# Kernel tuning notes

Hardware: AMD Instinct MI355X
Metric: run time of the kernel (lower is better)

## Reference

```python
import jax, jax.numpy as jnp
import numpy as np

N_NODES = 50000
N_EDGES = 800000
D_FEAT = 128
D_EMB = 128


def setup_inputs() -> dict:
    key = jax.random.key(0)
    k1, k2, k3, k4, k5 = jax.random.split(key, 5)
    feature = jax.random.normal(k1, (N_NODES, D_FEAT), dtype=jnp.float32)
    edge_src = jax.random.randint(k2, (N_EDGES,), 0, N_NODES, dtype=jnp.int32)
    edge_dst = jax.random.randint(k3, (N_EDGES,), 0, N_NODES, dtype=jnp.int32)
    edge_w = jax.random.uniform(k4, (N_EDGES,), dtype=jnp.float32)
    # reset_parameters: uniform(-stdv, stdv), stdv = 1/sqrt(embedding_size)
    stdv = 1.0 / np.sqrt(D_EMB)
    weight = jax.random.uniform(k5, (D_FEAT, D_EMB), dtype=jnp.float32,
                                minval=-stdv, maxval=stdv)
    return {"feature": feature, "edge_src": edge_src, "edge_dst": edge_dst,
            "edge_w": edge_w, "weight": weight}


def reference(feature, edge_src, edge_dst, edge_w, weight):
    # spmm(adj, feature): out[dst] += w * feature[src]
    msgs = edge_w[:, None] * feature[edge_src]          # [E, D_FEAT]
    agg = jax.ops.segment_sum(msgs, edge_dst, num_segments=feature.shape[0])
    # residual blend then dense projection
    blended = 0.5 * agg + 0.5 * feature                  # [N, D_FEAT]
    return blended @ weight                              # [N, D_EMB]
```

## Files before the change

kernel.cpp:

```cpp
#include <hip/hip_runtime.h>

#define N_NODES 50000
#define N_EDGES 800000
#define D 128
#define NBUCK 196
#define CAP 4800
#define CHUNK 2048

typedef __attribute__((ext_vector_type(8))) short short8;
typedef __attribute__((ext_vector_type(4))) float f32x4;

__device__ __forceinline__ unsigned short f2bf(float f) {
    unsigned u = __float_as_uint(f);
    u += 0x7fff + ((u >> 16) & 1);
    return (unsigned short)(u >> 16);
}

__global__ __launch_bounds__(256) void prep(const float2* __restrict__ feat2,
                                            unsigned* __restrict__ fb,
                                            const float* __restrict__ W,
                                            unsigned short* __restrict__ Wt,
                                            int* __restrict__ gcur) {
    int blk = blockIdx.x, t = threadIdx.x;
    if (blk < 12500) {
        int i = blk * 256 + t;
        float2 f = feat2[i];
        fb[i] = (unsigned)f2bf(f.x) | ((unsigned)f2bf(f.y) << 16);
    } else if (blk < 12564) {
        int idx = (blk - 12500) * 256 + t;
        int n = idx >> 7, k = idx & 127;
        Wt[idx] = f2bf(W[k * 128 + n]);
    } else {
        if (t < NBUCK) gcur[t] = 0;
    }
}

__global__ __launch_bounds__(256) void passA(const int* __restrict__ esrc,
                                             const int* __restrict__ edst,
                                             const float* __restrict__ ew,
                                             int* __restrict__ gcur,
                                             uint2* __restrict__ tmp) {
    __shared__ int lh[NBUCK], lbase[NBUCK], lcur[NBUCK];
    int t = threadIdx.x;
    for (int i = t; i < NBUCK; i += 256) lh[i] = 0;
    __syncthreads();

    int e0 = blockIdx.x * CHUNK;
    int s[8], d[8];
    float w[8];
#pragma unroll
    for (int j = 0; j < 8; ++j) {
        int e = e0 + j * 256 + t;
        if (e < N_EDGES) {
            s[j] = esrc[e]; d[j] = edst[e]; w[j] = ew[e];
            atomicAdd(&lh[d[j] >> 8], 1);
        } else d[j] = -1;
    }
    __syncthreads();
    for (int i = t; i < NBUCK; i += 256) {
        lbase[i] = atomicAdd(&gcur[i], lh[i]);
        lcur[i] = 0;
    }
    __syncthreads();
#pragma unroll
    for (int j = 0; j < 8; ++j) {
        if (d[j] >= 0) {
            int b = d[j] >> 8;
            int r = atomicAdd(&lcur[b], 1);
            tmp[(size_t)b * CAP + lbase[b] + r] =
                make_uint2((unsigned)s[j] | ((unsigned)(d[j] & 255) << 16),
                           __float_as_uint(w[j]));
        }
    }
}

__global__ __launch_bounds__(256) void passB(const int* __restrict__ gcur,
                                             const uint2* __restrict__ tmp,
                                             int* __restrict__ offsets,
                                             uint2* __restrict__ sw) {
    __shared__ int gb[NBUCK];
    __shared__ int hist[256], ps[256];
    __shared__ int sbase;
    int b = blockIdx.x, t = threadIdx.x;
    for (int i = t; i < NBUCK; i += 256) gb[i] = gcur[i];
    hist[t] = 0;
    __syncthreads();
    if (t == 0) {
        int run = 0;
        for (int i = 0; i < b; ++i) run += gb[i];
        sbase = run;
    }
    __syncthreads();
    int base = sbase, cnt = gb[b];
    const uint2* seg = tmp + (size_t)b * CAP;

    for (int i = t; i < cnt; i += 256) atomicAdd(&hist[seg[i].x >> 16], 1);
    __syncthreads();
    int h = hist[t];
    ps[t] = h;
    __syncthreads();
    for (int off = 1; off < 256; off <<= 1) {
        int x = (t >= off) ? ps[t - off] : 0;
        __syncthreads();
        ps[t] += x;
        __syncthreads();
    }
    int o = base + ps[t] - h;
    int node = b * 256 + t;
    if (node < N_NODES) offsets[node] = o;
    if (b == NBUCK - 1 && t == 0) offsets[N_NODES] = N_EDGES;
    __syncthreads();
    hist[t] = o;
    __syncthreads();
    for (int i = t; i < cnt; i += 256) {
        uint2 u = seg[i];
        int pos = atomicAdd(&hist[u.x >> 16], 1);
        sw[pos] = make_uint2(u.x & 0xffffu, u.y);
    }
}

__global__ __launch_bounds__(256) void aggregate_bf16(const int* __restrict__ offsets,
                                                      const uint2* __restrict__ sw,
                                                      const unsigned* __restrict__ fb,
                                                      float* __restrict__ out) {
    int n = blockIdx.x * 4 + (threadIdx.x >> 6);
    n = __builtin_amdgcn_readfirstlane(n);
    int lane = threadIdx.x & 63;
    int b = offsets[n], e2 = offsets[n + 1];
    float ax = 0.f, ay = 0.f;
    int e = b;
    for (; e + 4 <= e2; e += 4) {
        uint2 p0 = sw[e], p1 = sw[e + 1], p2 = sw[e + 2], p3 = sw[e + 3];
        unsigned u0 = fb[(size_t)p0.x * 64 + lane];
        unsigned u1 = fb[(size_t)p1.x * 64 + lane];
        unsigned u2 = fb[(size_t)p2.x * 64 + lane];
        unsigned u3 = fb[(size_t)p3.x * 64 + lane];
        float w0 = __uint_as_float(p0.y), w1 = __uint_as_float(p1.y);
        float w2 = __uint_as_float(p2.y), w3 = __uint_as_float(p3.y);
        ax += w0 * __uint_as_float(u0 << 16);
        ay += w0 * __uint_as_float(u0 & 0xffff0000u);
        ax += w1 * __uint_as_float(u1 << 16);
        ay += w1 * __uint_as_float(u1 & 0xffff0000u);
        ax += w2 * __uint_as_float(u2 << 16);
        ay += w2 * __uint_as_float(u2 & 0xffff0000u);
        ax += w3 * __uint_as_float(u3 << 16);
        ay += w3 * __uint_as_float(u3 & 0xffff0000u);
    }
    for (; e < e2; ++e) {
        uint2 p = sw[e];
        unsigned u = fb[(size_t)p.x * 64 + lane];
        float w = __uint_as_float(p.y);
        ax += w * __uint_as_float(u << 16);
        ay += w * __uint_as_float(u & 0xffff0000u);
    }
    unsigned us = fb[(size_t)n * 64 + lane];
    float sx = __uint_as_float(us << 16), sy = __uint_as_float(us & 0xffff0000u);
    ((float2*)out)[(size_t)n * 64 + lane] = make_float2(0.5f * (ax + sx), 0.5f * (ay + sy));
}

__global__ __launch_bounds__(256) void gemm_mfma_inplace(const unsigned short* __restrict__ Wt,
                                                         float* __restrict__ out) {
    int wave = threadIdx.x >> 6;
    int lane = threadIdx.x & 63;
    int quad = lane >> 4;
    int col  = lane & 15;
    int m0 = blockIdx.x * 64 + wave * 16;
    int rowA = m0 + col;
    int r = rowA < N_NODES ? rowA : N_NODES - 1;
    const float* rp = out + (size_t)r * D;

    short8 a[4];
#pragma unroll
    for (int kk = 0; kk < 4; ++kk) {
        int k0 = kk * 32 + quad * 8;
        float4 lo = *reinterpret_cast<const float4*>(rp + k0);
        float4 hi = *reinterpret_cast<const float4*>(rp + k0 + 4);
        short8 av;
        av[0] = (short)f2bf(lo.x); av[1] = (short)f2bf(lo.y);
        av[2] = (short)f2bf(lo.z); av[3] = (short)f2bf(lo.w);
        av[4] = (short)f2bf(hi.x); av[5] = (short)f2bf(hi.y);
        av[6] = (short)f2bf(hi.z); av[7] = (short)f2bf(hi.w);
        a[kk] = av;
    }

#pragma unroll
    for (int n0 = 0; n0 < 8; ++n0) {
        const short8* bp = reinterpret_cast<const short8*>(Wt) + ((n0 * 16 + col) * 16 + quad);
        f32x4 acc = {0.f, 0.f, 0.f, 0.f};
        acc = __builtin_amdgcn_mfma_f32_16x16x32_bf16(a[0], bp[0],  acc, 0, 0, 0);
        acc = __builtin_amdgcn_mfma_f32_16x16x32_bf16(a[1], bp[4],  acc, 0, 0, 0);
        acc = __builtin_amdgcn_mfma_f32_16x16x32_bf16(a[2], bp[8],  acc, 0, 0, 0);
        acc = __builtin_amdgcn_mfma_f32_16x16x32_bf16(a[3], bp[12], acc, 0, 0, 0);
#pragma unroll
        for (int rr = 0; rr < 4; ++rr) {
            int grow = m0 + quad * 4 + rr;
            if (grow < N_NODES) out[(size_t)grow * D + n0 * 16 + col] = acc[rr];
        }
    }
}

extern "C" void kernel_launch(void* const* d_in, const int* in_sizes, int n_in,
                              void* d_out, int out_size, void* d_ws, size_t ws_size,
                              hipStream_t stream) {
    const float* feat = (const float*)d_in[0];
    const int*   esrc = (const int*)d_in[1];
    const int*   edst = (const int*)d_in[2];
    const float* ew   = (const float*)d_in[3];
    const float* W    = (const float*)d_in[4];
    float*       out  = (float*)d_out;

    char* ws = (char*)d_ws;
    uint2*          sw      = (uint2*)(ws + 0);
    unsigned*       fb      = (unsigned*)(ws + 6400000);
    int*            offsets = (int*)(ws + 19200000);
    unsigned short* Wt      = (unsigned short*)(ws + 19400064);
    int*            gcur    = (int*)(ws + 19432832);
    uint2* tmp = (uint2*)d_out;

    prep<<<12565, 256, 0, stream>>>((const float2*)feat, fb, W, Wt, gcur);
    passA<<<(N_EDGES + CHUNK - 1) / CHUNK, 256, 0, stream>>>(esrc, edst, ew, gcur, tmp);
    passB<<<NBUCK, 256, 0, stream>>>(gcur, tmp, offsets, sw);
    aggregate_bf16<<<N_NODES / 4, 256, 0, stream>>>(offsets, sw, fb, out);
    gemm_mfma_inplace<<<(N_NODES + 63) / 64, 256, 0, stream>>>(Wt, out);
}
```

Before: 170.2 us.

## Fuse aggregation with MFMA projection and merge prep into bucketing pass

Aggregation and the bf16 MFMA projection are merged into one kernel. Each block aggregates 16 rows into an LDS tile as bf16, then four waves each compute two 16-column output tiles, so the fp32 intermediate no longer makes a round trip through global memory. The prep and passA kernels are merged into one launch, with counter zeroing moved to a memset, and the gather loop is unrolled to 8 edges for more loads in flight. In exchange there is less parallelism per row in the aggregation, and each block has to wait at a barrier before its projection can start.

```diff
diff --git a/kernel.cpp b/kernel.cpp
--- a/kernel.cpp
+++ b/kernel.cpp
@@ -6,6 +6,9 @@
 #define NBUCK 196
 #define CAP 4800
 #define CHUNK 2048
+#define PA_BLKS ((N_EDGES + CHUNK - 1) / CHUNK)
+#define FB_BLKS 12500
+#define WT_BLKS 64
 
 typedef __attribute__((ext_vector_type(8))) short short8;
 typedef __attribute__((ext_vector_type(4))) float f32x4;
@@ -16,36 +19,32 @@
     return (unsigned short)(u >> 16);
 }
 
-__global__ __launch_bounds__(256) void prep(const float2* __restrict__ feat2,
-                                            unsigned* __restrict__ fb,
-                                            const float* __restrict__ W,
-                                            unsigned short* __restrict__ Wt,
-                                            int* __restrict__ gcur) {
+__global__ __launch_bounds__(256) void prep_passA(
+    const float2* __restrict__ feat2, unsigned* __restrict__ fb,
+    const float* __restrict__ W, unsigned short* __restrict__ Wt,
+    const int* __restrict__ esrc, const int* __restrict__ edst,
+    const float* __restrict__ ew, int* __restrict__ gcur,
+    uint2* __restrict__ tmp) {
+    __shared__ int lh[NBUCK], lbase[NBUCK], lcur[NBUCK];
     int blk = blockIdx.x, t = threadIdx.x;
-    if (blk < 12500) {
-        int i = blk * 256 + t;
-        float2 f = feat2[i];
-        fb[i] = (unsigned)f2bf(f.x) | ((unsigned)f2bf(f.y) << 16);
-    } else if (blk < 12564) {
-        int idx = (blk - 12500) * 256 + t;
-        int n = idx >> 7, k = idx & 127;
-        Wt[idx] = f2bf(W[k * 128 + n]);
-    } else {
-        if (t < NBUCK) gcur[t] = 0;
-    }
-}
-
-__global__ __launch_bounds__(256) void passA(const int* __restrict__ esrc,
-                                             const int* __restrict__ edst,
-                                             const float* __restrict__ ew,
-                                             int* __restrict__ gcur,
-                                             uint2* __restrict__ tmp) {
-    __shared__ int lh[NBUCK], lbase[NBUCK], lcur[NBUCK];
-    int t = threadIdx.x;
+
+    if (blk >= PA_BLKS) {
+        int b2 = blk - PA_BLKS;
+        if (b2 < FB_BLKS) {
+            int i = b2 * 256 + t;
+            float2 f = feat2[i];
+            fb[i] = (unsigned)f2bf(f.x) | ((unsigned)f2bf(f.y) << 16);
+        } else {
+            int idx = (b2 - FB_BLKS) * 256 + t;
+            int n = idx >> 7, k = idx & 127;
+            Wt[idx] = f2bf(W[k * 128 + n]);
+        }
+        return;
+    }
+
     for (int i = t; i < NBUCK; i += 256) lh[i] = 0;
     __syncthreads();
-
-    int e0 = blockIdx.x * CHUNK;
+    int e0 = blk * CHUNK;
     int s[8], d[8];
     float w[8];
 #pragma unroll
@@ -119,72 +118,61 @@
     }
 }
 
-__global__ __launch_bounds__(256) void aggregate_bf16(const int* __restrict__ offsets,
-                                                      const uint2* __restrict__ sw,
-                                                      const unsigned* __restrict__ fb,
-                                                      float* __restrict__ out) {
-    int n = blockIdx.x * 4 + (threadIdx.x >> 6);
-    n = __builtin_amdgcn_readfirstlane(n);
-    int lane = threadIdx.x & 63;
-    int b = offsets[n], e2 = offsets[n + 1];
-    float ax = 0.f, ay = 0.f;
-    int e = b;
-    for (; e + 4 <= e2; e += 4) {
-        uint2 p0 = sw[e], p1 = sw[e + 1], p2 = sw[e + 2], p3 = sw[e + 3];
-        unsigned u0 = fb[(size_t)p0.x * 64 + lane];
-        unsigned u1 = fb[(size_t)p1.x * 64 + lane];
-        unsigned u2 = fb[(size_t)p2.x * 64 + lane];
-        unsigned u3 = fb[(size_t)p3.x * 64 + lane];
-        float w0 = __uint_as_float(p0.y), w1 = __uint_as_float(p1.y);
-        float w2 = __uint_as_float(p2.y), w3 = __uint_as_float(p3.y);
-        ax += w0 * __uint_as_float(u0 << 16);
-        ay += w0 * __uint_as_float(u0 & 0xffff0000u);
-        ax += w1 * __uint_as_float(u1 << 16);
-        ay += w1 * __uint_as_float(u1 & 0xffff0000u);
-        ax += w2 * __uint_as_float(u2 << 16);
-        ay += w2 * __uint_as_float(u2 & 0xffff0000u);
-        ax += w3 * __uint_as_float(u3 << 16);
-        ay += w3 * __uint_as_float(u3 & 0xffff0000u);
-    }
-    for (; e < e2; ++e) {
-        uint2 p = sw[e];
-        unsigned u = fb[(size_t)p.x * 64 + lane];
-        float w = __uint_as_float(p.y);
-        ax += w * __uint_as_float(u << 16);
-        ay += w * __uint_as_float(u & 0xffff0000u);
-    }
-    unsigned us = fb[(size_t)n * 64 + lane];
-    float sx = __uint_as_float(us << 16), sy = __uint_as_float(us & 0xffff0000u);
-    ((float2*)out)[(size_t)n * 64 + lane] = make_float2(0.5f * (ax + sx), 0.5f * (ay + sy));
-}
-
-__global__ __launch_bounds__(256) void gemm_mfma_inplace(const unsigned short* __restrict__ Wt,
-                                                         float* __restrict__ out) {
+__global__ __launch_bounds__(256) void agg_gemm(const int* __restrict__ offsets,
+                                                const uint2* __restrict__ sw,
+                                                const unsigned* __restrict__ fb,
+                                                const unsigned short* __restrict__ Wt,
+                                                float* __restrict__ out) {
+    __shared__ unsigned Arows[16][68];
     int wave = threadIdx.x >> 6;
     int lane = threadIdx.x & 63;
+    int row0 = blockIdx.x * 16;
+
+#pragma unroll 1
+    for (int i = 0; i < 4; ++i) {
+        int n = row0 + wave * 4 + i;
+        n = __builtin_amdgcn_readfirstlane(n);
+        int b = offsets[n], e2 = offsets[n + 1];
+        float ax = 0.f, ay = 0.f;
+        int e = b;
+        for (; e + 8 <= e2; e += 8) {
+            uint2 p[8];
+            unsigned u[8];
+#pragma unroll
+            for (int j = 0; j < 8; ++j) p[j] = sw[e + j];
+#pragma unroll
+            for (int j = 0; j < 8; ++j) u[j] = fb[(size_t)p[j].x * 64 + lane];
+#pragma unroll
+            for (int j = 0; j < 8; ++j) {
+                float w = __uint_as_float(p[j].y);
+                ax += w * __uint_as_float(u[j] << 16);
+                ay += w * __uint_as_float(u[j] & 0xffff0000u);
+            }
+        }
+        for (; e < e2; ++e) {
+            uint2 p = sw[e];
+            unsigned u = fb[(size_t)p.x * 64 + lane];
+            float w = __uint_as_float(p.y);
+            ax += w * __uint_as_float(u << 16);
+            ay += w * __uint_as_float(u & 0xffff0000u);
+        }
+        unsigned us = fb[(size_t)n * 64 + lane];
+        float rx = 0.5f * (ax + __uint_as_float(us << 16));
+        float ry = 0.5f * (ay + __uint_as_float(us & 0xffff0000u));
+        Arows[wave * 4 + i][lane] = (unsigned)f2bf(rx) | ((unsigned)f2bf(ry) << 16);
+    }
+    __syncthreads();
+
     int quad = lane >> 4;
     int col  = lane & 15;
-    int m0 = blockIdx.x * 64 + wave * 16;
-    int rowA = m0 + col;
-    int r = rowA < N_NODES ? rowA : N_NODES - 1;
-    const float* rp = out + (size_t)r * D;
-
     short8 a[4];
 #pragma unroll
-    for (int kk = 0; kk < 4; ++kk) {
-        int k0 = kk * 32 + quad * 8;
-        float4 lo = *reinterpret_cast<const float4*>(rp + k0);
-        float4 hi = *reinterpret_cast<const float4*>(rp + k0 + 4);
-        short8 av;
-        av[0] = (short)f2bf(lo.x); av[1] = (short)f2bf(lo.y);
-        av[2] = (short)f2bf(lo.z); av[3] = (short)f2bf(lo.w);
-        av[4] = (short)f2bf(hi.x); av[5] = (short)f2bf(hi.y);
-        av[6] = (short)f2bf(hi.z); av[7] = (short)f2bf(hi.w);
-        a[kk] = av;
-    }
-
-#pragma unroll
-    for (int n0 = 0; n0 < 8; ++n0) {
+    for (int kk = 0; kk < 4; ++kk)
+        a[kk] = *reinterpret_cast<const short8*>(&Arows[col][kk * 16 + quad * 4]);
+
+#pragma unroll
+    for (int ii = 0; ii < 2; ++ii) {
+        int n0 = wave * 2 + ii;
         const short8* bp = reinterpret_cast<const short8*>(Wt) + ((n0 * 16 + col) * 16 + quad);
         f32x4 acc = {0.f, 0.f, 0.f, 0.f};
         acc = __builtin_amdgcn_mfma_f32_16x16x32_bf16(a[0], bp[0],  acc, 0, 0, 0);
@@ -192,10 +180,8 @@
         acc = __builtin_amdgcn_mfma_f32_16x16x32_bf16(a[2], bp[8],  acc, 0, 0, 0);
         acc = __builtin_amdgcn_mfma_f32_16x16x32_bf16(a[3], bp[12], acc, 0, 0, 0);
 #pragma unroll
-        for (int rr = 0; rr < 4; ++rr) {
-            int grow = m0 + quad * 4 + rr;
-            if (grow < N_NODES) out[(size_t)grow * D + n0 * 16 + col] = acc[rr];
-        }
+        for (int rr = 0; rr < 4; ++rr)
+            out[(size_t)(row0 + quad * 4 + rr) * D + n0 * 16 + col] = acc[rr];
     }
 }
 
@@ -217,9 +203,9 @@
     int*            gcur    = (int*)(ws + 19432832);
     uint2* tmp = (uint2*)d_out;
 
-    prep<<<12565, 256, 0, stream>>>((const float2*)feat, fb, W, Wt, gcur);
-    passA<<<(N_EDGES + CHUNK - 1) / CHUNK, 256, 0, stream>>>(esrc, edst, ew, gcur, tmp);
+    hipMemsetAsync(gcur, 0, NBUCK * sizeof(int), stream);
+    prep_passA<<<PA_BLKS + FB_BLKS + WT_BLKS, 256, 0, stream>>>(
+        (const float2*)feat, fb, W, Wt, esrc, edst, ew, gcur, tmp);
     passB<<<NBUCK, 256, 0, stream>>>(gcur, tmp, offsets, sw);
-    aggregate_bf16<<<N_NODES / 4, 256, 0, stream>>>(offsets, sw, fb, out);
-    gemm_mfma_inplace<<<(N_NODES + 63) / 64, 256, 0, stream>>>(Wt, out);
-}
+    agg_gemm<<<N_NODES / 16, 256, 0, stream>>>(offsets, sw, fb, Wt, out);
+}
```

Measured after the change: 157.2 us. 7.6% less time.
